# Kernel tuning notes

Hardware: AMD Instinct MI355X
Metric: run time of the kernel (lower is better)

## Reference

```python
import jax, jax.numpy as jnp
import numpy as np

B, C, H, W = 1, 64, 512, 512
OUT_CH = 1
EPS = 1e-5


def conv2d(x, w, b, pad):
    y = jax.lax.conv_general_dilated(
        x, w, window_strides=(1, 1), padding=[(pad, pad), (pad, pad)],
        dimension_numbers=("NCHW", "OIHW", "NCHW"))
    return y + b[None, :, None, None]


def _bilinear_one(xb, py, px):
    # xb: [C,H,W]; py, px: [H,W] fractional sample coords; zero padding outside.
    Ch, Hh, Wh = xb.shape
    y0 = jnp.floor(py)
    x0 = jnp.floor(px)
    wy = py - y0
    wx = px - x0
    y0i = y0.astype(jnp.int32)
    x0i = x0.astype(jnp.int32)
    xf = xb.reshape(Ch, -1)

    def g(yi, xi):
        valid = (yi >= 0) & (yi < Hh) & (xi >= 0) & (xi < Wh)
        yc = jnp.clip(yi, 0, Hh - 1)
        xc = jnp.clip(xi, 0, Wh - 1)
        idx = (yc * Wh + xc).reshape(-1)
        v = xf[:, idx].reshape(Ch, Hh, Wh)
        return v * valid[None].astype(xb.dtype)

    v00 = g(y0i, x0i)
    v01 = g(y0i, x0i + 1)
    v10 = g(y0i + 1, x0i)
    v11 = g(y0i + 1, x0i + 1)
    return (v00 * (1 - wy) * (1 - wx) + v01 * (1 - wy) * wx
            + v10 * wy * (1 - wx) + v11 * wy * wx)


_bilinear = jax.vmap(_bilinear_one, in_axes=(0, 0, 0))


def deform_conv2d(x, offset, weight, bias):
    # torchvision DeformConv2d semantics: offset [B, 2*K, H, W], (dy, dx) per
    # kernel tap in row-major order, kernel 3x3, pad 1, stride 1.
    b, cin, h, w = x.shape
    off = offset.reshape(b, 9, 2, h, w)
    ii = jnp.arange(h, dtype=x.dtype)[:, None]  # [H,1]
    jj = jnp.arange(w, dtype=x.dtype)[None, :]  # [1,W]
    acc = jnp.zeros((b, weight.shape[0], h, w), dtype=x.dtype)
    for k in range(9):  # fixed small loop over kernel taps
        ky, kx = k // 3, k % 3
        py = ii + (ky - 1) + off[:, k, 0]  # [B,H,W]
        px = jj + (kx - 1) + off[:, k, 1]
        s = _bilinear(x, py, px)  # [B,Cin,H,W]
        acc = acc + jnp.einsum("bchw,oc->bohw", s, weight[:, :, ky, kx])
    return acc + bias[None, :, None, None]


def batchnorm(x, gamma, beta, mean, var):
    inv = gamma * jax.lax.rsqrt(var + EPS)
    return x * inv[None, :, None, None] + (beta - mean * inv)[None, :, None, None]


def setup_inputs() -> dict:
    key = jax.random.key(0)
    ks = jax.random.split(key, 16)
    d = {
        "x": jax.random.normal(ks[0], (B, C, H, W), jnp.float32),
        "offset1_w": jax.random.normal(ks[1], (18, C, 3, 3), jnp.float32) * 0.01,
        "offset1_b": jnp.zeros((18,), jnp.float32),
        "dcn1_w": jax.random.normal(ks[2], (C, C, 3, 3), jnp.float32) * 0.05,
        "dcn1_b": jnp.zeros((C,), jnp.float32),
        "bn1_gamma": jnp.ones((C,), jnp.float32),
        "bn1_beta": jnp.zeros((C,), jnp.float32),
        "bn1_mean": jax.random.normal(ks[3], (C,), jnp.float32) * 0.1,
        "bn1_var": jax.random.uniform(ks[4], (C,), jnp.float32, 0.5, 1.5),
        "offset2_w": jax.random.normal(ks[5], (18, C, 3, 3), jnp.float32) * 0.01,
        "offset2_b": jnp.zeros((18,), jnp.float32),
        "dcn2_w": jax.random.normal(ks[6], (C, C, 3, 3), jnp.float32) * 0.05,
        "dcn2_b": jnp.zeros((C,), jnp.float32),
        "bn2_gamma": jnp.ones((C,), jnp.float32),
        "bn2_beta": jnp.zeros((C,), jnp.float32),
        "bn2_mean": jax.random.normal(ks[7], (C,), jnp.float32) * 0.1,
        "bn2_var": jax.random.uniform(ks[8], (C,), jnp.float32, 0.5, 1.5),
        "conv_w": jax.random.normal(ks[9], (OUT_CH, C, 1, 1), jnp.float32) * 0.1,
        "conv_b": jnp.zeros((OUT_CH,), jnp.float32),
    }
    return d


def reference(x, offset1_w, offset1_b, dcn1_w, dcn1_b, bn1_gamma, bn1_beta,
              bn1_mean, bn1_var, offset2_w, offset2_b, dcn2_w, dcn2_b,
              bn2_gamma, bn2_beta, bn2_mean, bn2_var, conv_w, conv_b):
    off1 = conv2d(x, offset1_w, offset1_b, pad=1)
    h = deform_conv2d(x, off1, dcn1_w, dcn1_b)
    h = jax.nn.relu(batchnorm(h, bn1_gamma, bn1_beta, bn1_mean, bn1_var))
    off2 = conv2d(h, offset2_w, offset2_b, pad=1)
    h = deform_conv2d(h, off2, dcn2_w, dcn2_b)
    h = jax.nn.relu(batchnorm(h, bn2_gamma, bn2_beta, bn2_mean, bn2_var))
    return conv2d(h, conv_w, conv_b, pad=0)
```

## Files before the change

kernel.cpp:

```cpp
#include <hip/hip_runtime.h>
#include <math.h>

#define HWSZ (512*512)
#define EPSV 1e-5f

typedef _Float16 h8 __attribute__((ext_vector_type(8)));
typedef _Float16 h4 __attribute__((ext_vector_type(4)));
typedef _Float16 h2 __attribute__((ext_vector_type(2)));
typedef float    f32x4 __attribute__((ext_vector_type(4)));

__device__ __forceinline__ h8 as_h8(uint4 u) { return __builtin_bit_cast(h8, u); }
__device__ __forceinline__ uint4 as_u4(h8 v) { return __builtin_bit_cast(uint4, v); }

__device__ __forceinline__ int xcd_swz_4096(int bid) {
    return (bid & 7) * 512 + (bid >> 3);
}

__global__ __launch_bounds__(256) void to_hwc_f16(const float* __restrict__ in,
                                                  unsigned* __restrict__ out32) {
    __shared__ float T[64 * 65];
    int tid = threadIdx.x;
    int pbase = blockIdx.x * 64;
    int p = tid & 63, cg = tid >> 6;
#pragma unroll
    for (int j = 0; j < 16; ++j) {
        int c = cg * 16 + j;
        T[p * 65 + c] = in[c * HWSZ + pbase + p];
    }
    __syncthreads();
    int px = tid >> 2, cb = (tid & 3) * 16;
#pragma unroll
    for (int j = 0; j < 8; ++j) {
        int c = cb + 2 * j;
        h2 v = {(_Float16)T[px * 65 + c], (_Float16)T[px * 65 + c + 1]};
        out32[(pbase + px) * 32 + (c >> 1)] = __builtin_bit_cast(unsigned, v);
    }
}

__global__ __launch_bounds__(256) void prep_all(
        const float* __restrict__ dw1, const float* __restrict__ dw2,
        const float* __restrict__ ow1, const float* __restrict__ ow2,
        _Float16* __restrict__ wT1, _Float16* __restrict__ wT2,
        _Float16* __restrict__ wTo1, _Float16* __restrict__ wTo2) {
    int i = blockIdx.x * 256 + threadIdx.x;
    if (i < 36864) {
        int k = i / 4096, r = i % 4096;
        int s = r >> 9, o = (r >> 3) & 63, j = r & 7;
        int c = (s >> 2) * 32 + (s & 3) * 8 + j;
        wT1[i] = (_Float16)dw1[(o * 64 + c) * 9 + k];
    } else if (i < 73728) {
        int ii = i - 36864;
        int k = ii / 4096, r = ii % 4096;
        int s = r >> 9, o = (r >> 3) & 63, j = r & 7;
        int c = (s >> 2) * 32 + (s & 3) * 8 + j;
        wT2[ii] = (_Float16)dw2[(o * 64 + c) * 9 + k];
    } else if (i < 92160) {
        int j = i - 73728;
        int k = j / 2048, r = j % 2048, o = r >> 6, c = r & 63;
        wTo1[k * 2048 + o * 64 + c] = (_Float16)((o < 18) ? ow1[(o * 64 + c) * 9 + k] : 0.f);
    } else if (i < 110592) {
        int j = i - 92160;
        int k = j / 2048, r = j % 2048, o = r >> 6, c = r & 63;
        wTo2[k * 2048 + o * 64 + c] = (_Float16)((o < 18) ? ow2[(o * 64 + c) * 9 + k] : 0.f);
    }
}

__global__ __launch_bounds__(256, 4) void conv3x3_off_mfma(
        const _Float16* __restrict__ in, const _Float16* __restrict__ wTo,
        const float* __restrict__ bias, _Float16* __restrict__ off) {
    __shared__ uint4 TILE[3 * 66 * 8];

    int tid = threadIdx.x;
    int pbase = xcd_swz_4096(blockIdx.x) * 64;
    int y = pbase >> 9, xblk = pbase & 511;
    int l = tid & 63, wv = tid >> 6;
    int lq = l & 15, quad = l >> 4;
    int wn = wv & 1, wm = wv >> 1;

    h8 breg[18];
#pragma unroll
    for (int k = 0; k < 9; ++k)
#pragma unroll
        for (int kc = 0; kc < 2; ++kc)
            breg[k * 2 + kc] = *(const h8*)(wTo + k * 2048 + (wn * 16 + lq) * 64 + kc * 32 + quad * 8);

    uint4 v[7];
#pragma unroll
    for (int i = 0; i < 7; ++i) {
        int t = tid + 256 * i;
        int row = t / 528, r = t - row * 528;
        int col = r >> 3, cc = r & 7;
        int sy = y + row - 1, sx = xblk + col - 1;
        bool ok = (t < 1584) && ((unsigned)sy < 512u) && ((unsigned)sx < 512u);
        v[i] = ok ? *(const uint4*)(in + (sy * 512 + sx) * 64 + cc * 8)
                  : make_uint4(0u, 0u, 0u, 0u);
    }
#pragma unroll
    for (int i = 0; i < 7; ++i) {
        int t = tid + 256 * i;
        if (t < 1584) {
            int row = t / 528, r = t - row * 528;
            int col = r >> 3, cc = r & 7;
            TILE[(row * 66 + col) * 8 + (cc ^ (col & 7))] = v[i];
        }
    }
    __syncthreads();

    f32x4 zero = {0.f, 0.f, 0.f, 0.f};
    f32x4 acc[2]; acc[0] = zero; acc[1] = zero;

#pragma unroll
    for (int k = 0; k < 9; ++k) {
        int ky = k / 3, kx = k % 3;
#pragma unroll
        for (int kc = 0; kc < 2; ++kc) {
#pragma unroll
            for (int tm = 0; tm < 2; ++tm) {
                int col = kx + wm * 32 + tm * 16 + lq;
                int cc0 = kc * 4 + quad;
                h8 a = as_h8(TILE[(ky * 66 + col) * 8 + (cc0 ^ (col & 7))]);
                acc[tm] = __builtin_amdgcn_mfma_f32_16x16x32_f16(a, breg[k * 2 + kc], acc[tm], 0, 0, 0);
            }
        }
    }

    int n = wn * 16 + lq;
    if (n < 18) {
        float bb = bias[n];
#pragma unroll
        for (int tm = 0; tm < 2; ++tm)
#pragma unroll
            for (int reg = 0; reg < 4; ++reg) {
                int px = wm * 32 + tm * 16 + quad * 4 + reg;
                off[(pbase + px) * 18 + n] = (_Float16)(acc[tm][reg] + bb);
            }
    }
}

__global__ __launch_bounds__(256, 3) void dcn_fused(
        const _Float16* __restrict__ in, const _Float16* __restrict__ off,
        const _Float16* __restrict__ wTd, const float* __restrict__ bias,
        const float* __restrict__ gamma, const float* __restrict__ beta,
        const float* __restrict__ mean, const float* __restrict__ var,
        _Float16* __restrict__ out) {
    __shared__ uint4  WIN[196 * 8];
    __shared__ h4     SW9[9 * 64];
    __shared__ short4 SI9[9 * 64];
    __shared__ float  scl_s[64], sh_s[64];

    int tid = threadIdx.x;
    int bid = blockIdx.x;
    int ty = bid >> 6, tx = bid & 63;
    int r0 = ty * 8, c0 = tx * 8;
    int wr0 = r0 - 3, wc0 = c0 - 3;

    for (int t = tid; t < 576; t += 256) {
        int p = t & 63, k = t >> 6;
        int pr = p >> 3, pc = p & 7;
        int y = r0 + pr, x = c0 + pc;
        int gp = y * 512 + x;
        h2 dv = *(const h2*)(off + gp * 18 + 2 * k);
        float py = (float)(y + k / 3 - 1) + (float)dv[0];
        float px = (float)(x + k % 3 - 1) + (float)dv[1];
        float y0f = floorf(py), x0f = floorf(px);
        float wy = py - y0f, wx = px - x0f;
        int y0 = (int)y0f, x0 = (int)x0f;
        int y1 = y0 + 1, x1 = x0 + 1;
        float vy0 = ((unsigned)y0 < 512u) ? 1.f : 0.f;
        float vy1 = ((unsigned)y1 < 512u) ? 1.f : 0.f;
        float vx0 = ((unsigned)x0 < 512u) ? 1.f : 0.f;
        float vx1 = ((unsigned)x1 < 512u) ? 1.f : 0.f;
        SW9[t] = (h4){(_Float16)((1.f - wy) * (1.f - wx) * vy0 * vx0),
                      (_Float16)((1.f - wy) * wx * vy0 * vx1),
                      (_Float16)(wy * (1.f - wx) * vy1 * vx0),
                      (_Float16)(wy * wx * vy1 * vx1)};
        int y0c = min(max(y0, 0), 511), y1c = min(max(y1, 0), 511);
        int x0c = min(max(x0, 0), 511), x1c = min(max(x1, 0), 511);
        SI9[t] = make_short4((short)(y0c - wr0), (short)(x0c - wc0),
                             (short)(y1c - wr0), (short)(x1c - wc0));
    }
    if (tid < 64) {
        float s = gamma[tid] * rsqrtf(var[tid] + EPSV);
        scl_s[tid] = s;
        sh_s[tid] = beta[tid] - mean[tid] * s + bias[tid] * s;
    }

    uint4 sv[7];
#pragma unroll
    for (int i = 0; i < 7; ++i) {
        int t = tid + 256 * i;
        int wp = t >> 3, cc = t & 7;
        int wi = wp / 14, wj = wp - wi * 14;
        int sy = wr0 + wi, sx = wc0 + wj;
        bool ok = (t < 1568) && ((unsigned)sy < 512u) && ((unsigned)sx < 512u);
        sv[i] = ok ? *(const uint4*)(in + ((sy << 9) + sx) * 64 + cc * 8)
                   : make_uint4(0u, 0u, 0u, 0u);
    }
#pragma unroll
    for (int i = 0; i < 7; ++i) {
        int t = tid + 256 * i;
        if (t < 1568) {
            int wp = t >> 3, cc = t & 7;
            WIN[wp * 8 + (cc ^ (wp & 7))] = sv[i];
        }
    }
    __syncthreads();

    int l = tid & 63, wv = tid >> 6;
    int lq = l & 15, quad = l >> 4;
    int pxl = wv * 16 + lq;

#define CORNER(LO, HI, WY, WX) do {                                           \
        int wy_ = (WY), wx_ = (WX);                                           \
        if ((unsigned)wy_ < 14u && (unsigned)wx_ < 14u) {                     \
            int wp_ = wy_ * 14 + wx_;                                         \
            int sw_ = wp_ & 7;                                                \
            LO = as_h8(WIN[wp_ * 8 + (quad ^ sw_)]);                          \
            HI = as_h8(WIN[wp_ * 8 + ((quad + 4) ^ sw_)]);                    \
        } else {                                                              \
            int iy_ = wy_ + wr0, ix_ = wx_ + wc0;                             \
            const _Float16* g_ = in + ((iy_ << 9) + ix_) * 64 + quad * 8;     \
            LO = *(const h8*)g_;                                              \
            HI = *(const h8*)(g_ + 32);                                       \
        }                                                                     \
    } while (0)

    f32x4 zero = {0.f, 0.f, 0.f, 0.f};
    f32x4 acc[4];
    acc[0] = zero; acc[1] = zero; acc[2] = zero; acc[3] = zero;

#pragma unroll
    for (int k = 0; k < 9; ++k) {
        const _Float16* wk = wTd + k * 4096;
        h8 bl[4], bh[4];
#pragma unroll
        for (int nb = 0; nb < 4; ++nb) {
            bl[nb] = *(const h8*)(wk + (quad * 64 + nb * 16 + lq) * 8);
            bh[nb] = *(const h8*)(wk + ((quad + 4) * 64 + nb * 16 + lq) * 8);
        }
        short4 s = SI9[k * 64 + pxl];
        h4 w = SW9[k * 64 + pxl];
        h8 c0l, c0h, c1l, c1h, c2l, c2h, c3l, c3h;
        CORNER(c0l, c0h, (int)s.x, (int)s.y);
        CORNER(c1l, c1h, (int)s.x, (int)s.w);
        CORNER(c2l, c2h, (int)s.z, (int)s.y);
        CORNER(c3l, c3h, (int)s.z, (int)s.w);
        h8 alo = c0l * w[0] + c1l * w[1] + c2l * w[2] + c3l * w[3];
        h8 ahi = c0h * w[0] + c1h * w[1] + c2h * w[2] + c3h * w[3];
#pragma unroll
        for (int nb = 0; nb < 4; ++nb)
            acc[nb] = __builtin_amdgcn_mfma_f32_16x16x32_f16(alo, bl[nb], acc[nb], 0, 0, 0);
#pragma unroll
        for (int nb = 0; nb < 4; ++nb)
            acc[nb] = __builtin_amdgcn_mfma_f32_16x16x32_f16(ahi, bh[nb], acc[nb], 0, 0, 0);
    }
#undef CORNER

#pragma unroll
    for (int nb = 0; nb < 4; ++nb) {
        float sc = scl_s[nb * 16 + lq];
        float sh = sh_s[nb * 16 + lq];
#pragma unroll
        for (int reg = 0; reg < 4; ++reg) {
            int p_out = wv * 16 + quad * 4 + reg;
            int gp = (r0 + (p_out >> 3)) * 512 + c0 + (p_out & 7);
            out[gp * 64 + nb * 16 + lq] =
                (_Float16)fmaxf(fmaf(acc[nb][reg], sc, sh), 0.f);
        }
    }
}

__global__ __launch_bounds__(256) void conv1x1_out(const _Float16* __restrict__ in,
                                                   const float* __restrict__ w,
                                                   const float* __restrict__ b,
                                                   float* __restrict__ out) {
    int p = blockIdx.x * 256 + threadIdx.x;
    float acc = b[0];
    const h8* ip = (const h8*)(in + p * 64);
#pragma unroll
    for (int j = 0; j < 8; ++j) {
        h8 v = ip[j];
#pragma unroll
        for (int e = 0; e < 8; ++e)
            acc = fmaf((float)v[e], w[j * 8 + e], acc);
    }
    out[p] = acc;
}

extern "C" void kernel_launch(void* const* d_in, const int* in_sizes, int n_in,
                              void* d_out, int out_size, void* d_ws, size_t ws_size,
                              hipStream_t stream) {
    const float* x      = (const float*)d_in[0];
    const float* off1_w = (const float*)d_in[1];
    const float* off1_b = (const float*)d_in[2];
    const float* dcn1_w = (const float*)d_in[3];
    const float* dcn1_b = (const float*)d_in[4];
    const float* bn1_g  = (const float*)d_in[5];
    const float* bn1_be = (const float*)d_in[6];
    const float* bn1_m  = (const float*)d_in[7];
    const float* bn1_v  = (const float*)d_in[8];
    const float* off2_w = (const float*)d_in[9];
    const float* off2_b = (const float*)d_in[10];
    const float* dcn2_w = (const float*)d_in[11];
    const float* dcn2_b = (const float*)d_in[12];
    const float* bn2_g  = (const float*)d_in[13];
    const float* bn2_be = (const float*)d_in[14];
    const float* bn2_m  = (const float*)d_in[15];
    const float* bn2_v  = (const float*)d_in[16];
    const float* conv_w = (const float*)d_in[17];
    const float* conv_b = (const float*)d_in[18];
    float* out = (float*)d_out;

    char* ws = (char*)d_ws;
    _Float16* xh   = (_Float16*)ws;
    _Float16* h1   = (_Float16*)(ws + 33554432);
    _Float16* offb = (_Float16*)(ws + 2 * 33554432);
    _Float16* wT1  = (_Float16*)(ws + 2 * 33554432 + 9437184);
    _Float16* wT2  = wT1 + 36864;
    _Float16* wTo1 = wT2 + 36864;
    _Float16* wTo2 = wTo1 + 18432;
    _Float16* h2 = xh;

    prep_all<<<432, 256, 0, stream>>>(dcn1_w, dcn2_w, off1_w, off2_w,
                                      wT1, wT2, wTo1, wTo2);
    to_hwc_f16<<<4096, 256, 0, stream>>>(x, (unsigned*)xh);

    conv3x3_off_mfma<<<4096, 256, 0, stream>>>(xh, wTo1, off1_b, offb);
    dcn_fused<<<4096, 256, 0, stream>>>(xh, offb, wT1, dcn1_b,
                                        bn1_g, bn1_be, bn1_m, bn1_v, h1);
    conv3x3_off_mfma<<<4096, 256, 0, stream>>>(h1, wTo2, off2_b, offb);
    dcn_fused<<<4096, 256, 0, stream>>>(h1, offb, wT2, dcn2_b,
                                        bn2_g, bn2_be, bn2_m, bn2_v, h2);
    conv1x1_out<<<1024, 256, 0, stream>>>(h2, conv_w, conv_b, out);
}
```

Before: 322.0 us.

## Fuse final 1x1 conv into second DCN and precompute per-tap corner addressing

The final 1x1 output convolution is folded into the second deformable-conv kernel's epilogue. Each lane forms its partial dot product over its channels and the result is reduced with 16-lane shuffles, so the 32MB fp16 intermediate is never written and read back and one launch disappears. The sampling setup also precomputes a window index plus flags for the in-window case, replacing four per-corner bounds checks with a single branch that takes either all-LDS or all-global loads. This adds shuffle work to the epilogue and changes the corner-loading control flow.

```diff
diff --git a/kernel.cpp b/kernel.cpp
--- a/kernel.cpp
+++ b/kernel.cpp
@@ -137,12 +137,15 @@
     }
 }
 
+template<int FINAL>
 __global__ __launch_bounds__(256, 3) void dcn_fused(
         const _Float16* __restrict__ in, const _Float16* __restrict__ off,
         const _Float16* __restrict__ wTd, const float* __restrict__ bias,
         const float* __restrict__ gamma, const float* __restrict__ beta,
         const float* __restrict__ mean, const float* __restrict__ var,
-        _Float16* __restrict__ out) {
+        _Float16* __restrict__ out,
+        const float* __restrict__ w1x1, const float* __restrict__ b1x1,
+        float* __restrict__ outf) {
     __shared__ uint4  WIN[196 * 8];
     __shared__ h4     SW9[9 * 64];
     __shared__ short4 SI9[9 * 64];
@@ -176,8 +179,15 @@
                       (_Float16)(wy * wx * vy1 * vx1)};
         int y0c = min(max(y0, 0), 511), y1c = min(max(y1, 0), 511);
         int x0c = min(max(x0, 0), 511), x1c = min(max(x1, 0), 511);
-        SI9[t] = make_short4((short)(y0c - wr0), (short)(x0c - wc0),
-                             (short)(y1c - wr0), (short)(x1c - wc0));
+        int wy0 = y0c - wr0, wx0 = x0c - wc0;
+        int wy1 = y1c - wr0, wx1 = x1c - wc0;
+        int dx = x1c - x0c;
+        int dyf = (y1c != y0c) ? 2 : 0;
+        bool inwin = ((unsigned)wy0 < 14u) && ((unsigned)wy1 < 14u) &&
+                     ((unsigned)wx0 < 14u) && ((unsigned)wx1 < 14u);
+        int flags = dx | dyf | (inwin ? 4 : 0);
+        SI9[t] = make_short4((short)(wy0 * 14 + wx0), (short)flags,
+                             (short)y0c, (short)x0c);
     }
     if (tid < 64) {
         float s = gamma[tid] * rsqrtf(var[tid] + EPSV);
@@ -209,21 +219,8 @@
     int l = tid & 63, wv = tid >> 6;
     int lq = l & 15, quad = l >> 4;
     int pxl = wv * 16 + lq;
-
-#define CORNER(LO, HI, WY, WX) do {                                           \
-        int wy_ = (WY), wx_ = (WX);                                           \
-        if ((unsigned)wy_ < 14u && (unsigned)wx_ < 14u) {                     \
-            int wp_ = wy_ * 14 + wx_;                                         \
-            int sw_ = wp_ & 7;                                                \
-            LO = as_h8(WIN[wp_ * 8 + (quad ^ sw_)]);                          \
-            HI = as_h8(WIN[wp_ * 8 + ((quad + 4) ^ sw_)]);                    \
-        } else {                                                              \
-            int iy_ = wy_ + wr0, ix_ = wx_ + wc0;                             \
-            const _Float16* g_ = in + ((iy_ << 9) + ix_) * 64 + quad * 8;     \
-            LO = *(const h8*)g_;                                              \
-            HI = *(const h8*)(g_ + 32);                                       \
-        }                                                                     \
-    } while (0)
+    const char* Wb = (const char*)WIN;
+    int qsl = quad << 4;
 
     f32x4 zero = {0.f, 0.f, 0.f, 0.f};
     f32x4 acc[4];
@@ -241,10 +238,31 @@
         short4 s = SI9[k * 64 + pxl];
         h4 w = SW9[k * 64 + pxl];
         h8 c0l, c0h, c1l, c1h, c2l, c2h, c3l, c3h;
-        CORNER(c0l, c0h, (int)s.x, (int)s.y);
-        CORNER(c1l, c1h, (int)s.x, (int)s.w);
-        CORNER(c2l, c2h, (int)s.z, (int)s.y);
-        CORNER(c3l, c3h, (int)s.z, (int)s.w);
+        if (s.y & 4) {
+            int dx  = s.y & 1;
+            int dy  = (s.y & 2) ? 14 : 0;
+            int wp0 = s.x;
+            int wp1 = wp0 + dx, wp2 = wp0 + dy, wp3 = wp2 + dx;
+            int b0 = (wp0 << 7) + (((quad ^ (wp0 & 7))) << 4);
+            int b1 = (wp1 << 7) + (((quad ^ (wp1 & 7))) << 4);
+            int b2 = (wp2 << 7) + (((quad ^ (wp2 & 7))) << 4);
+            int b3 = (wp3 << 7) + (((quad ^ (wp3 & 7))) << 4);
+            c0l = *(const h8*)(Wb + b0); c0h = *(const h8*)(Wb + (b0 ^ 64));
+            c1l = *(const h8*)(Wb + b1); c1h = *(const h8*)(Wb + (b1 ^ 64));
+            c2l = *(const h8*)(Wb + b2); c2h = *(const h8*)(Wb + (b2 ^ 64));
+            c3l = *(const h8*)(Wb + b3); c3h = *(const h8*)(Wb + (b3 ^ 64));
+        } else {
+            int dx = s.y & 1, dyr = (s.y >> 1) & 1;
+            int y0c = s.z, x0c = s.w;
+            const _Float16* g00 = in + (((y0c) << 9) + x0c) * 64 + quad * 8;
+            const _Float16* g01 = in + (((y0c) << 9) + x0c + dx) * 64 + quad * 8;
+            const _Float16* g10 = in + (((y0c + dyr) << 9) + x0c) * 64 + quad * 8;
+            const _Float16* g11 = in + (((y0c + dyr) << 9) + x0c + dx) * 64 + quad * 8;
+            c0l = *(const h8*)g00; c0h = *(const h8*)(g00 + 32);
+            c1l = *(const h8*)g01; c1h = *(const h8*)(g01 + 32);
+            c2l = *(const h8*)g10; c2h = *(const h8*)(g10 + 32);
+            c3l = *(const h8*)g11; c3h = *(const h8*)(g11 + 32);
+        }
         h8 alo = c0l * w[0] + c1l * w[1] + c2l * w[2] + c3l * w[3];
         h8 ahi = c0h * w[0] + c1h * w[1] + c2h * w[2] + c3h * w[3];
 #pragma unroll
@@ -254,37 +272,46 @@
         for (int nb = 0; nb < 4; ++nb)
             acc[nb] = __builtin_amdgcn_mfma_f32_16x16x32_f16(ahi, bh[nb], acc[nb], 0, 0, 0);
     }
-#undef CORNER
-
+
+    float sc[4], sh[4];
 #pragma unroll
     for (int nb = 0; nb < 4; ++nb) {
-        float sc = scl_s[nb * 16 + lq];
-        float sh = sh_s[nb * 16 + lq];
+        sc[nb] = scl_s[nb * 16 + lq];
+        sh[nb] = sh_s[nb * 16 + lq];
+    }
+    if constexpr (FINAL) {
+        float wv4[4];
+#pragma unroll
+        for (int nb = 0; nb < 4; ++nb) wv4[nb] = w1x1[nb * 16 + lq];
+        float bb = b1x1[0];
 #pragma unroll
         for (int reg = 0; reg < 4; ++reg) {
-            int p_out = wv * 16 + quad * 4 + reg;
-            int gp = (r0 + (p_out >> 3)) * 512 + c0 + (p_out & 7);
-            out[gp * 64 + nb * 16 + lq] =
-                (_Float16)fmaxf(fmaf(acc[nb][reg], sc, sh), 0.f);
-        }
-    }
-}
-
-__global__ __launch_bounds__(256) void conv1x1_out(const _Float16* __restrict__ in,
-                                                   const float* __restrict__ w,
-                                                   const float* __restrict__ b,
-                                                   float* __restrict__ out) {
-    int p = blockIdx.x * 256 + threadIdx.x;
-    float acc = b[0];
-    const h8* ip = (const h8*)(in + p * 64);
-#pragma unroll
-    for (int j = 0; j < 8; ++j) {
-        h8 v = ip[j];
-#pragma unroll
-        for (int e = 0; e < 8; ++e)
-            acc = fmaf((float)v[e], w[j * 8 + e], acc);
-    }
-    out[p] = acc;
+            float v = 0.f;
+#pragma unroll
+            for (int nb = 0; nb < 4; ++nb)
+                v += fmaxf(fmaf(acc[nb][reg], sc[nb], sh[nb]), 0.f) * wv4[nb];
+            v += __shfl_xor(v, 1, 16);
+            v += __shfl_xor(v, 2, 16);
+            v += __shfl_xor(v, 4, 16);
+            v += __shfl_xor(v, 8, 16);
+            if (lq == 0) {
+                int p_out = wv * 16 + quad * 4 + reg;
+                int gp = (r0 + (p_out >> 3)) * 512 + c0 + (p_out & 7);
+                outf[gp] = v + bb;
+            }
+        }
+    } else {
+#pragma unroll
+        for (int nb = 0; nb < 4; ++nb) {
+#pragma unroll
+            for (int reg = 0; reg < 4; ++reg) {
+                int p_out = wv * 16 + quad * 4 + reg;
+                int gp = (r0 + (p_out >> 3)) * 512 + c0 + (p_out & 7);
+                out[gp * 64 + nb * 16 + lq] =
+                    (_Float16)fmaxf(fmaf(acc[nb][reg], sc[nb], sh[nb]), 0.f);
+            }
+        }
+    }
 }
 
 extern "C" void kernel_launch(void* const* d_in, const int* in_sizes, int n_in,
@@ -319,17 +346,17 @@
     _Float16* wT2  = wT1 + 36864;
     _Float16* wTo1 = wT2 + 36864;
     _Float16* wTo2 = wTo1 + 18432;
-    _Float16* h2 = xh;
 
     prep_all<<<432, 256, 0, stream>>>(dcn1_w, dcn2_w, off1_w, off2_w,
                                       wT1, wT2, wTo1, wTo2);
     to_hwc_f16<<<4096, 256, 0, stream>>>(x, (unsigned*)xh);
 
     conv3x3_off_mfma<<<4096, 256, 0, stream>>>(xh, wTo1, off1_b, offb);
-    dcn_fused<<<4096, 256, 0, stream>>>(xh, offb, wT1, dcn1_b,
-                                        bn1_g, bn1_be, bn1_m, bn1_v, h1);
+    dcn_fused<0><<<4096, 256, 0, stream>>>(xh, offb, wT1, dcn1_b,
+                                           bn1_g, bn1_be, bn1_m, bn1_v, h1,
+                                           nullptr, nullptr, nullptr);
     conv3x3_off_mfma<<<4096, 256, 0, stream>>>(h1, wTo2, off2_b, offb);
-    dcn_fused<<<4096, 256, 0, stream>>>(h1, offb, wT2, dcn2_b,
-                                        bn2_g, bn2_be, bn2_m, bn2_v, h2);
-    conv1x1_out<<<1024, 256, 0, stream>>>(h2, conv_w, conv_b, out);
-}
+    dcn_fused<1><<<4096, 256, 0, stream>>>(h1, offb, wT2, dcn2_b,
+                                           bn2_g, bn2_be, bn2_m, bn2_v, nullptr,
+                                           conv_w, conv_b, out);
+}
```

New measurement: 363.4 us. +12.9%, slower.

## Split DCN work by output-channel waves with register-resident weights and double-buffered LDS samples

Applied to the files above, without the earlier changes.

The fused deformable conv kernel changes its work split. Before, each wave blended all 64 channels for its own 16 pixels and reloaded the full weight tile from global memory on every tap. Now each wave blends a 16-channel slice for all 64 pixels into a double-buffered LDS sample buffer, and each wave owns 16 output channels whose weights for all 9 taps stay in registers. The next tap's blend overlaps the current tap's MFMAs, and the weight prep layout changes to match. The cost is more register pressure from the 18 h8 weight registers, extra LDS space and a barrier per tap.

```diff
diff --git a/kernel.cpp b/kernel.cpp
--- a/kernel.cpp
+++ b/kernel.cpp
@@ -11,6 +11,10 @@
 
 __device__ __forceinline__ h8 as_h8(uint4 u) { return __builtin_bit_cast(h8, u); }
 __device__ __forceinline__ uint4 as_u4(h8 v) { return __builtin_bit_cast(uint4, v); }
+
+__device__ __forceinline__ void lds_barrier() {
+    asm volatile("s_waitcnt lgkmcnt(0)\n\ts_barrier" ::: "memory");
+}
 
 __device__ __forceinline__ int xcd_swz_4096(int bid) {
     return (bid & 7) * 512 + (bid >> 3);
@@ -44,16 +48,12 @@
         _Float16* __restrict__ wTo1, _Float16* __restrict__ wTo2) {
     int i = blockIdx.x * 256 + threadIdx.x;
     if (i < 36864) {
-        int k = i / 4096, r = i % 4096;
-        int s = r >> 9, o = (r >> 3) & 63, j = r & 7;
-        int c = (s >> 2) * 32 + (s & 3) * 8 + j;
-        wT1[i] = (_Float16)dw1[(o * 64 + c) * 9 + k];
+        int k = i / 4096, r = i % 4096, o = r >> 6, c = r & 63;
+        wT1[k * 4096 + o * 64 + c] = (_Float16)dw1[(o * 64 + c) * 9 + k];
     } else if (i < 73728) {
-        int ii = i - 36864;
-        int k = ii / 4096, r = ii % 4096;
-        int s = r >> 9, o = (r >> 3) & 63, j = r & 7;
-        int c = (s >> 2) * 32 + (s & 3) * 8 + j;
-        wT2[ii] = (_Float16)dw2[(o * 64 + c) * 9 + k];
+        int j = i - 36864;
+        int k = j / 4096, r = j % 4096, o = r >> 6, c = r & 63;
+        wT2[k * 4096 + o * 64 + c] = (_Float16)dw2[(o * 64 + c) * 9 + k];
     } else if (i < 92160) {
         int j = i - 73728;
         int k = j / 2048, r = j % 2048, o = r >> 6, c = r & 63;
@@ -144,6 +144,7 @@
         const float* __restrict__ mean, const float* __restrict__ var,
         _Float16* __restrict__ out) {
     __shared__ uint4  WIN[196 * 8];
+    __shared__ uint4  SBUF[2][512];
     __shared__ h4     SW9[9 * 64];
     __shared__ short4 SI9[9 * 64];
     __shared__ float  scl_s[64], sh_s[64];
@@ -153,6 +154,17 @@
     int ty = bid >> 6, tx = bid & 63;
     int r0 = ty * 8, c0 = tx * 8;
     int wr0 = r0 - 3, wc0 = c0 - 3;
+
+    int l = tid & 63, wv = tid >> 6;
+    int lq = l & 15, quad = l >> 4;
+
+    h8 breg[18];
+#pragma unroll
+    for (int k = 0; k < 9; ++k) {
+        const _Float16* wk = wTd + k * 4096 + (wv * 16 + lq) * 64;
+        breg[k * 2 + 0] = *(const h8*)(wk + quad * 8);
+        breg[k * 2 + 1] = *(const h8*)(wk + 32 + quad * 8);
+    }
 
     for (int t = tid; t < 576; t += 256) {
         int p = t & 63, k = t >> 6;
@@ -206,66 +218,73 @@
     }
     __syncthreads();
 
-    int l = tid & 63, wv = tid >> 6;
-    int lq = l & 15, quad = l >> 4;
-    int pxl = wv * 16 + lq;
-
-#define CORNER(LO, HI, WY, WX) do {                                           \
+    int bpx = tid & 63, cg = tid >> 6;
+    int s0 = 2 * cg, s1 = 2 * cg + 1;
+    int cg16 = cg * 16;
+
+#define CORNER(A, B, WY, WX) do {                                             \
         int wy_ = (WY), wx_ = (WX);                                           \
         if ((unsigned)wy_ < 14u && (unsigned)wx_ < 14u) {                     \
             int wp_ = wy_ * 14 + wx_;                                         \
             int sw_ = wp_ & 7;                                                \
-            LO = as_h8(WIN[wp_ * 8 + (quad ^ sw_)]);                          \
-            HI = as_h8(WIN[wp_ * 8 + ((quad + 4) ^ sw_)]);                    \
+            A = as_h8(WIN[wp_ * 8 + (s0 ^ sw_)]);                             \
+            B = as_h8(WIN[wp_ * 8 + (s1 ^ sw_)]);                             \
         } else {                                                              \
-            int iy_ = wy_ + wr0, ix_ = wx_ + wc0;                             \
-            const _Float16* g_ = in + ((iy_ << 9) + ix_) * 64 + quad * 8;     \
-            LO = *(const h8*)g_;                                              \
-            HI = *(const h8*)(g_ + 32);                                       \
+            const _Float16* g_ = in + (((wy_ + wr0) << 9) + wx_ + wc0) * 64 + cg16; \
+            A = *(const h8*)g_;                                               \
+            B = *(const h8*)(g_ + 8);                                         \
         }                                                                     \
+    } while (0)
+
+#define BLEND(K, BUF) do {                                                    \
+        short4 s_ = SI9[(K) * 64 + bpx];                                      \
+        h4 w_ = SW9[(K) * 64 + bpx];                                          \
+        h8 q0a, q0b, q1a, q1b, q2a, q2b, q3a, q3b;                            \
+        CORNER(q0a, q0b, s_.x, s_.y);                                         \
+        CORNER(q1a, q1b, s_.x, s_.w);                                         \
+        CORNER(q2a, q2b, s_.z, s_.y);                                         \
+        CORNER(q3a, q3b, s_.z, s_.w);                                         \
+        h8 lo_ = q0a * w_[0] + q1a * w_[1] + q2a * w_[2] + q3a * w_[3];       \
+        h8 hi_ = q0b * w_[0] + q1b * w_[1] + q2b * w_[2] + q3b * w_[3];       \
+        SBUF[BUF][bpx * 8 + (s0 ^ (bpx & 7))] = as_u4(lo_);                   \
+        SBUF[BUF][bpx * 8 + (s1 ^ (bpx & 7))] = as_u4(hi_);                   \
     } while (0)
 
     f32x4 zero = {0.f, 0.f, 0.f, 0.f};
     f32x4 acc[4];
     acc[0] = zero; acc[1] = zero; acc[2] = zero; acc[3] = zero;
 
+    BLEND(0, 0);
+    lds_barrier();
+
 #pragma unroll
     for (int k = 0; k < 9; ++k) {
-        const _Float16* wk = wTd + k * 4096;
-        h8 bl[4], bh[4];
-#pragma unroll
-        for (int nb = 0; nb < 4; ++nb) {
-            bl[nb] = *(const h8*)(wk + (quad * 64 + nb * 16 + lq) * 8);
-            bh[nb] = *(const h8*)(wk + ((quad + 4) * 64 + nb * 16 + lq) * 8);
-        }
-        short4 s = SI9[k * 64 + pxl];
-        h4 w = SW9[k * 64 + pxl];
-        h8 c0l, c0h, c1l, c1h, c2l, c2h, c3l, c3h;
-        CORNER(c0l, c0h, (int)s.x, (int)s.y);
-        CORNER(c1l, c1h, (int)s.x, (int)s.w);
-        CORNER(c2l, c2h, (int)s.z, (int)s.y);
-        CORNER(c3l, c3h, (int)s.z, (int)s.w);
-        h8 alo = c0l * w[0] + c1l * w[1] + c2l * w[2] + c3l * w[3];
-        h8 ahi = c0h * w[0] + c1h * w[1] + c2h * w[2] + c3h * w[3];
-#pragma unroll
-        for (int nb = 0; nb < 4; ++nb)
-            acc[nb] = __builtin_amdgcn_mfma_f32_16x16x32_f16(alo, bl[nb], acc[nb], 0, 0, 0);
-#pragma unroll
-        for (int nb = 0; nb < 4; ++nb)
-            acc[nb] = __builtin_amdgcn_mfma_f32_16x16x32_f16(ahi, bh[nb], acc[nb], 0, 0, 0);
+        int cur = k & 1;
+        if (k < 8) BLEND(k + 1, cur ^ 1);
+        h8 bA = breg[k * 2 + 0], bB = breg[k * 2 + 1];
+#pragma unroll
+        for (int g = 0; g < 4; ++g) {
+            int apx = g * 16 + lq;
+            h8 alo = as_h8(SBUF[cur][apx * 8 + (quad ^ (apx & 7))]);
+            h8 ahi = as_h8(SBUF[cur][apx * 8 + ((quad + 4) ^ (apx & 7))]);
+            acc[g] = __builtin_amdgcn_mfma_f32_16x16x32_f16(alo, bA, acc[g], 0, 0, 0);
+            acc[g] = __builtin_amdgcn_mfma_f32_16x16x32_f16(ahi, bB, acc[g], 0, 0, 0);
+        }
+        lds_barrier();
     }
 #undef CORNER
-
-#pragma unroll
-    for (int nb = 0; nb < 4; ++nb) {
-        float sc = scl_s[nb * 16 + lq];
-        float sh = sh_s[nb * 16 + lq];
+#undef BLEND
+
+    float sc = scl_s[wv * 16 + lq];
+    float sh = sh_s[wv * 16 + lq];
+#pragma unroll
+    for (int g = 0; g < 4; ++g) {
 #pragma unroll
         for (int reg = 0; reg < 4; ++reg) {
-            int p_out = wv * 16 + quad * 4 + reg;
+            int p_out = g * 16 + quad * 4 + reg;
             int gp = (r0 + (p_out >> 3)) * 512 + c0 + (p_out & 7);
-            out[gp * 64 + nb * 16 + lq] =
-                (_Float16)fmaxf(fmaf(acc[nb][reg], sc, sh), 0.f);
+            out[gp * 64 + wv * 16 + lq] =
+                (_Float16)fmaxf(fmaf(acc[g][reg], sc, sh), 0.f);
         }
     }
 }
```

Measured after the change: 379.4 us. +17.8%, slower.
